# Kernel optimization log

Measured on AMD Instinct MI355X. Metric: run time of the kernel, lower is better.

## Reference

```python
import jax, jax.numpy as jnp
import numpy as np


def setup_inputs() -> dict:
    key = jax.random.key(0)
    k1, k2 = jax.random.split(key)
    D, N, M = 256, 1024, 1024
    z_x = jax.random.normal(k1, (1, D, N), dtype=jnp.float32)
    z_y = jax.random.normal(k2, (1, D, M), dtype=jnp.float32)
    return {"z_x": z_x, "z_y": z_y}


def reference(z_x, z_y):
    # squeeze().t(): (1, d, N) -> (N, d)
    x = jnp.squeeze(z_x).T  # (N, d)
    y = jnp.squeeze(z_y).T  # (M, d)
    # L1 compare: s[i, j] = -sum_d |x[i, d] - y[j, d]|  -> (N, M)
    s = -jnp.sum(jnp.abs(x[:, None, :] - y[None, :, :]), axis=-1)
    a = jax.nn.softmax(s, axis=1)  # row-wise softmax
    b = jax.nn.softmax(s, axis=0)  # column-wise softmax
    a = a + b - a * b              # soft union of alignments
    return jnp.sum(a * s) / jnp.sum(a)
```

## Files before the change

kernel.cpp:

```cpp
#include <hip/hip_runtime.h>
#include <math.h>


#define DD 256
#define NN 1024
#define NQ 256

__device__ __forceinline__ float waveMax(float v) {
  #pragma unroll
  for (int off = 32; off; off >>= 1) v = fmaxf(v, __shfl_xor(v, off, 64));
  return v;
}
__device__ __forceinline__ float waveSum(float v) {
  #pragma unroll
  for (int off = 32; off; off >>= 1) v += __shfl_xor(v, off, 64);
  return v;
}


__global__ __launch_bounds__(256, 1)
void scompute_kernel(const float* __restrict__ zx, const float* __restrict__ zy,
                     float* __restrict__ S,
                     float* __restrict__ pRM, float* __restrict__ pRL,
                     float* __restrict__ pCM, float* __restrict__ pCL) {
  const int bx = blockIdx.x;
  const int by = blockIdx.y;
  const int i0 = by * 16;
  const int t  = threadIdx.x;
  const int w  = t >> 6;
  const int ln = t & 63;

  __shared__ float xs[DD][16];
  __shared__ float ys[2][8][256];
  __shared__ float cmS[4][256];
  __shared__ float clS[4][256];

  const float4* __restrict__ X4 = (const float4*)zx;
  const float4* __restrict__ Y4 = (const float4*)zy;

  #pragma unroll
  for (int i = 0; i < 4; ++i) {
    const int k = t + i * 256;
    const int d = k >> 2, rq = k & 3;
    *(float4*)&xs[d][rq * 4] = X4[d * NQ + by * 4 + rq];
  }

  const int sd = t >> 6;
  const int sq = t & 63;
  {
    const float4 q0 = Y4[(sd)     * NQ + bx * 64 + sq];
    const float4 q1 = Y4[(4 + sd) * NQ + bx * 64 + sq];
    *(float4*)&ys[0][sd][sq * 4]     = q0;
    *(float4*)&ys[0][4 + sd][sq * 4] = q1;
  }
  __syncthreads();

  float acc[4][4];
  #pragma unroll
  for (int r = 0; r < 4; ++r)
    #pragma unroll
    for (int c = 0; c < 4; ++c) acc[r][c] = 0.f;

  #pragma unroll 1
  for (int n = 0; n < DD / 8; ++n) {
    const int buf = n & 1;
    float4 p0, p1;
    if (n < DD / 8 - 1) {
      p0 = Y4[(8 * (n + 1) + sd)     * NQ + bx * 64 + sq];
      p1 = Y4[(8 * (n + 1) + 4 + sd) * NQ + bx * 64 + sq];
    }
    #pragma unroll
    for (int dd = 0; dd < 8; ++dd) {
      const int d = n * 8 + dd;
      const float4 xv = *(const float4*)&xs[d][w * 4];
      const float4 yv = *(const float4*)&ys[buf][dd][ln * 4];
      acc[0][0] += fabsf(xv.x - yv.x); acc[0][1] += fabsf(xv.x - yv.y);
      acc[0][2] += fabsf(xv.x - yv.z); acc[0][3] += fabsf(xv.x - yv.w);
      acc[1][0] += fabsf(xv.y - yv.x); acc[1][1] += fabsf(xv.y - yv.y);
      acc[1][2] += fabsf(xv.y - yv.z); acc[1][3] += fabsf(xv.y - yv.w);
      acc[2][0] += fabsf(xv.z - yv.x); acc[2][1] += fabsf(xv.z - yv.y);
      acc[2][2] += fabsf(xv.z - yv.z); acc[2][3] += fabsf(xv.z - yv.w);
      acc[3][0] += fabsf(xv.w - yv.x); acc[3][1] += fabsf(xv.w - yv.y);
      acc[3][2] += fabsf(xv.w - yv.z); acc[3][3] += fabsf(xv.w - yv.w);
    }
    if (n < DD / 8 - 1) {
      *(float4*)&ys[buf ^ 1][sd][sq * 4]     = p0;
      *(float4*)&ys[buf ^ 1][4 + sd][sq * 4] = p1;
    }
    __syncthreads();
  }

  float4* __restrict__ S4 = (float4*)S;
  #pragma unroll
  for (int r = 0; r < 4; ++r)
    S4[(i0 + w * 4 + r) * NQ + bx * 64 + ln] =
        make_float4(acc[r][0], acc[r][1], acc[r][2], acc[r][3]);

  #pragma unroll
  for (int r = 0; r < 4; ++r) {
    float m = fmaxf(fmaxf(-acc[r][0], -acc[r][1]), fmaxf(-acc[r][2], -acc[r][3]));
    m = waveMax(m);
    float l = __expf(-acc[r][0] - m) + __expf(-acc[r][1] - m) +
              __expf(-acc[r][2] - m) + __expf(-acc[r][3] - m);
    l = waveSum(l);
    if (ln == 0) {
      pRM[bx * NN + i0 + w * 4 + r] = m;
      pRL[bx * NN + i0 + w * 4 + r] = l;
    }
  }

  #pragma unroll
  for (int c = 0; c < 4; ++c) {
    float m = fmaxf(fmaxf(-acc[0][c], -acc[1][c]), fmaxf(-acc[2][c], -acc[3][c]));
    float l = __expf(-acc[0][c] - m) + __expf(-acc[1][c] - m) +
              __expf(-acc[2][c] - m) + __expf(-acc[3][c] - m);
    cmS[w][ln * 4 + c] = m;
    clS[w][ln * 4 + c] = l;
  }
  __syncthreads();
  {
    const int j = t;
    const float m0 = cmS[0][j], m1 = cmS[1][j], m2 = cmS[2][j], m3 = cmS[3][j];
    const float M = fmaxf(fmaxf(m0, m1), fmaxf(m2, m3));
    const float L = clS[0][j] * __expf(m0 - M) + clS[1][j] * __expf(m1 - M) +
                    clS[2][j] * __expf(m2 - M) + clS[3][j] * __expf(m3 - M);
    pCM[by * NN + bx * 256 + j] = M;
    pCL[by * NN + bx * 256 + j] = L;
  }
}

__global__ __launch_bounds__(256)
void combine_kernel(const float* __restrict__ pRM, const float* __restrict__ pRL,
                    const float* __restrict__ pCM, const float* __restrict__ pCL,
                    float* __restrict__ rmax, float* __restrict__ rsum,
                    float* __restrict__ cmax, float* __restrict__ csum,
                    float* __restrict__ accum) {
  const int b = blockIdx.x, t = threadIdx.x;
  if (b == 0 && t == 0) {
    accum[0] = 0.f; accum[1] = 0.f; ((unsigned int*)accum)[2] = 0u;
  }
  if (b < 4) {
    const int r = b * 256 + t;
    float mk[4], lk[4];
    #pragma unroll
    for (int k = 0; k < 4; ++k) { mk[k] = pRM[k * NN + r]; lk[k] = pRL[k * NN + r]; }
    float m = fmaxf(fmaxf(mk[0], mk[1]), fmaxf(mk[2], mk[3]));
    float l = lk[0] * __expf(mk[0] - m) + lk[1] * __expf(mk[1] - m) +
              lk[2] * __expf(mk[2] - m) + lk[3] * __expf(mk[3] - m);
    rmax[r] = m; rsum[r] = l;
  } else {
    const int j = (b - 4) * 256 + t;
    float m = -1e30f;
    #pragma unroll 8
    for (int k = 0; k < 64; ++k) m = fmaxf(m, pCM[k * NN + j]);
    float l = 0.f;
    #pragma unroll 8
    for (int k = 0; k < 64; ++k) l += __expf(pCM[k * NN + j] - m) * pCL[k * NN + j];
    cmax[j] = m; csum[j] = l;
  }
}

__global__ __launch_bounds__(256)
void final_kernel(const float* __restrict__ S,
                  const float* __restrict__ rmax, const float* __restrict__ rsum,
                  const float* __restrict__ cmax, const float* __restrict__ csum,
                  float* __restrict__ accum, float* __restrict__ out) {
  __shared__ float redn[4], redd[4];
  const int t = threadIdx.x;
  const int row0 = blockIdx.x * 2;
  const float4* S4 = (const float4*)S;
  const float4 cm = ((const float4*)cmax)[t];
  const float4 cs = ((const float4*)csum)[t];
  float un = 0.f, ud = 0.f;
  #pragma unroll
  for (int r = 0; r < 2; ++r) {
    const int row = row0 + r;
    const float rm = rmax[row];
    const float ri = 1.f / rsum[row];
    const float4 p = S4[row * NQ + t];
    {
      const float s = -p.x;
      const float a = __expf(s - rm) * ri;
      const float b = __expf(s - cm.x) / cs.x;
      const float u = a + b - a * b;
      un += u * s; ud += u;
    }
    {
      const float s = -p.y;
      const float a = __expf(s - rm) * ri;
      const float b = __expf(s - cm.y) / cs.y;
      const float u = a + b - a * b;
      un += u * s; ud += u;
    }
    {
      const float s = -p.z;
      const float a = __expf(s - rm) * ri;
      const float b = __expf(s - cm.z) / cs.z;
      const float u = a + b - a * b;
      un += u * s; ud += u;
    }
    {
      const float s = -p.w;
      const float a = __expf(s - rm) * ri;
      const float b = __expf(s - cm.w) / cs.w;
      const float u = a + b - a * b;
      un += u * s; ud += u;
    }
  }
  un = waveSum(un); ud = waveSum(ud);
  if ((t & 63) == 0) { redn[t >> 6] = un; redd[t >> 6] = ud; }
  __syncthreads();
  if (t == 0) {
    atomicAdd(&accum[0], redn[0] + redn[1] + redn[2] + redn[3]);
    atomicAdd(&accum[1], redd[0] + redd[1] + redd[2] + redd[3]);
    __threadfence();
    unsigned int* cnt = (unsigned int*)accum + 2;
    const unsigned int old = atomicAdd(cnt, 1u);
    if (old == gridDim.x - 1) {
      const float n = atomicAdd(&accum[0], 0.f);
      const float d = atomicAdd(&accum[1], 0.f);
      out[0] = n / d;
    }
  }
}


#define TJ  128
#define NCH (NN / TJ)
#define BLK 256

__global__ __launch_bounds__(BLK)
void stats2_kernel(const float* __restrict__ zx, const float* __restrict__ zy,
                   float* __restrict__ partM, float* __restrict__ partS) {
  const int side = blockIdx.z;
  const float* __restrict__ X = side ? zy : zx;
  const float* __restrict__ Y = side ? zx : zy;
  const int j0 = blockIdx.x * TJ;
  const int i0 = blockIdx.y * 8;
  const int t  = threadIdx.x;
  const int rg = t >> 5;
  const int c  = t & 31;

  __shared__ float xs[8 * DD];
  for (int k = t; k < 8 * DD; k += BLK)
    xs[k] = X[(k >> 3) * NN + i0 + (k & 7)];
  __syncthreads();

  const float4* __restrict__ Y4 = (const float4*)Y;
  const int yb = (j0 >> 2) + c;
  float4 acc = make_float4(0.f, 0.f, 0.f, 0.f);
  #pragma unroll 8
  for (int d = 0; d < DD; ++d) {
    const float4 yv = Y4[d * NQ + yb];
    const float xv = xs[d * 8 + rg];
    acc.x += fabsf(xv - yv.x);
    acc.y += fabsf(xv - yv.y);
    acc.z += fabsf(xv - yv.z);
    acc.w += fabsf(xv - yv.w);
  }

  float m = fmaxf(fmaxf(-acc.x, -acc.y), fmaxf(-acc.z, -acc.w));
  #pragma unroll
  for (int off = 16; off > 0; off >>= 1) m = fmaxf(m, __shfl_xor(m, off, 32));
  float p = __expf(-acc.x - m) + __expf(-acc.y - m) +
            __expf(-acc.z - m) + __expf(-acc.w - m);
  #pragma unroll
  for (int off = 16; off > 0; off >>= 1) p += __shfl_xor(p, off, 32);

  if (c == 0) {
    const int idx = side * (NCH * NN) + blockIdx.x * NN + (i0 + rg);
    partM[idx] = m;
    partS[idx] = p;
  }
}

__global__ __launch_bounds__(BLK)
void combine_kernel_fb(const float* __restrict__ partM, const float* __restrict__ partS,
                       float* __restrict__ rmax, float* __restrict__ rsum,
                       float* __restrict__ cmax, float* __restrict__ csum,
                       float* __restrict__ accum) {
  const int gid = blockIdx.x * BLK + threadIdx.x;
  if (gid == 0) { accum[0] = 0.f; accum[1] = 0.f; }
  const int sd = gid >> 10;
  const int i  = gid & (NN - 1);
  float mk[NCH], sk[NCH];
  #pragma unroll
  for (int k = 0; k < NCH; ++k) {
    mk[k] = partM[sd * (NCH * NN) + k * NN + i];
    sk[k] = partS[sd * (NCH * NN) + k * NN + i];
  }
  float m = mk[0];
  #pragma unroll
  for (int k = 1; k < NCH; ++k) m = fmaxf(m, mk[k]);
  float s = 0.f;
  #pragma unroll
  for (int k = 0; k < NCH; ++k) s += __expf(mk[k] - m) * sk[k];
  if (sd == 0) { rmax[i] = m; rsum[i] = s; }
  else         { cmax[i] = m; csum[i] = s; }
}

__global__ __launch_bounds__(BLK)
void final2_kernel(const float* __restrict__ zx, const float* __restrict__ zy,
                   const float* __restrict__ rmax, const float* __restrict__ rsum,
                   const float* __restrict__ cmax, const float* __restrict__ csum,
                   float* __restrict__ accum) {
  const int j0 = blockIdx.x * TJ;
  const int i0 = blockIdx.y * 8;
  const int t  = threadIdx.x;
  const int rg = t >> 5;
  const int c  = t & 31;

  __shared__ float xs[8 * DD];
  __shared__ float redn[4], redd[4];
  for (int k = t; k < 8 * DD; k += BLK)
    xs[k] = zx[(k >> 3) * NN + i0 + (k & 7)];
  __syncthreads();

  const float4* __restrict__ Y4 = (const float4*)zy;
  const int yb = (j0 >> 2) + c;
  float4 acc = make_float4(0.f, 0.f, 0.f, 0.f);
  #pragma unroll 8
  for (int d = 0; d < DD; ++d) {
    const float4 yv = Y4[d * NQ + yb];
    const float xv = xs[d * 8 + rg];
    acc.x += fabsf(xv - yv.x);
    acc.y += fabsf(xv - yv.y);
    acc.z += fabsf(xv - yv.z);
    acc.w += fabsf(xv - yv.w);
  }

  const int i = i0 + rg;
  const float rm = rmax[i];
  const float ri = 1.f / rsum[i];
  const float4 cm = ((const float4*)cmax)[yb];
  const float4 cs = ((const float4*)csum)[yb];

  float un = 0.f, ud = 0.f;
  {
    const float s = -acc.x;
    const float a = __expf(s - rm) * ri;
    const float b = __expf(s - cm.x) / cs.x;
    const float u = a + b - a * b;
    un += u * s; ud += u;
  }
  {
    const float s = -acc.y;
    const float a = __expf(s - rm) * ri;
    const float b = __expf(s - cm.y) / cs.y;
    const float u = a + b - a * b;
    un += u * s; ud += u;
  }
  {
    const float s = -acc.z;
    const float a = __expf(s - rm) * ri;
    const float b = __expf(s - cm.z) / cs.z;
    const float u = a + b - a * b;
    un += u * s; ud += u;
  }
  {
    const float s = -acc.w;
    const float a = __expf(s - rm) * ri;
    const float b = __expf(s - cm.w) / cs.w;
    const float u = a + b - a * b;
    un += u * s; ud += u;
  }

  un = waveSum(un); ud = waveSum(ud);
  if ((t & 63) == 0) { redn[t >> 6] = un; redd[t >> 6] = ud; }
  __syncthreads();
  if (t == 0) {
    atomicAdd(&accum[0], redn[0] + redn[1] + redn[2] + redn[3]);
    atomicAdd(&accum[1], redd[0] + redd[1] + redd[2] + redd[3]);
  }
}

__global__ void finalize_kernel(const float* __restrict__ accum, float* __restrict__ out) {
  out[0] = accum[0] / accum[1];
}


extern "C" void kernel_launch(void* const* d_in, const int* in_sizes, int n_in,
                              void* d_out, int out_size, void* d_ws, size_t ws_size,
                              hipStream_t stream) {
  const float* zx = (const float*)d_in[0];
  const float* zy = (const float*)d_in[1];
  float* ws  = (float*)d_ws;
  float* out = (float*)d_out;

  float* accum = ws;
  float* S     = ws + 16;
  float* pRM   = S + NN * NN;
  float* pRL   = pRM + 4 * NN;
  float* pCM   = pRL + 4 * NN;
  float* pCL   = pCM + 64 * NN;
  float* rmax  = pCL + 64 * NN;
  float* rsum  = rmax + NN;
  float* cmax  = rsum + NN;
  float* csum  = cmax + NN;
  const size_t need = (size_t)((csum + NN) - ws) * sizeof(float);

  if (ws_size >= need) {
    dim3 g1(4, 64);
    scompute_kernel<<<g1, 256, 0, stream>>>(zx, zy, S, pRM, pRL, pCM, pCL);
    combine_kernel<<<8, 256, 0, stream>>>(pRM, pRL, pCM, pCL,
                                          rmax, rsum, cmax, csum, accum);
    final_kernel<<<NN / 2, 256, 0, stream>>>(S, rmax, rsum, cmax, csum, accum, out);
  } else {
    float* partM = ws + 16;
    float* partS = partM + 2 * NCH * NN;
    float* frmax = partS + 2 * NCH * NN;
    float* frsum = frmax + NN;
    float* fcmax = frsum + NN;
    float* fcsum = fcmax + NN;
    dim3 sgrid(NCH, NN / 8, 2);
    stats2_kernel<<<sgrid, BLK, 0, stream>>>(zx, zy, partM, partS);
    combine_kernel_fb<<<(2 * NN) / BLK, BLK, 0, stream>>>(partM, partS,
                                                          frmax, frsum, fcmax, fcsum, accum);
    dim3 fgrid(NCH, NN / 8);
    final2_kernel<<<fgrid, BLK, 0, stream>>>(zx, zy, frmax, frsum, fcmax, fcsum, accum);
    finalize_kernel<<<1, 1, 0, stream>>>(accum, out);
  }
}
```

Before: 127.8 us.

## Split feature dimension across two grid slices and move softmax stats to separate pass

The S computation now splits the 256-wide feature dimension into two halves via a z grid dimension, doubling the block count from 256 to 512 so more CUs are busy. Each half writes a partial S matrix. Row and column softmax statistics move out of the compute kernel into a new sumstats kernel that sums the two partials, with a new column-combine kernel. This costs an extra full S-sized buffer, extra global read/write traffic, and one more launch.

```diff
diff --git a/kernel.cpp b/kernel.cpp
--- a/kernel.cpp
+++ b/kernel.cpp
@@ -5,6 +5,7 @@
 #define DD 256
 #define NN 1024
 #define NQ 256
+#define HD 128
 
 __device__ __forceinline__ float waveMax(float v) {
   #pragma unroll
@@ -16,43 +17,51 @@
   for (int off = 32; off; off >>= 1) v += __shfl_xor(v, off, 64);
   return v;
 }
-
-
-__global__ __launch_bounds__(256, 1)
+__device__ __forceinline__ float blockMax(float v, float* red) {
+  v = waveMax(v);
+  __syncthreads();
+  if ((threadIdx.x & 63) == 0) red[threadIdx.x >> 6] = v;
+  __syncthreads();
+  return fmaxf(fmaxf(red[0], red[1]), fmaxf(red[2], red[3]));
+}
+__device__ __forceinline__ float blockSum(float v, float* red) {
+  v = waveSum(v);
+  __syncthreads();
+  if ((threadIdx.x & 63) == 0) red[threadIdx.x >> 6] = v;
+  __syncthreads();
+  return red[0] + red[1] + red[2] + red[3];
+}
+
+
+__global__ __launch_bounds__(256, 2)
 void scompute_kernel(const float* __restrict__ zx, const float* __restrict__ zy,
-                     float* __restrict__ S,
-                     float* __restrict__ pRM, float* __restrict__ pRL,
-                     float* __restrict__ pCM, float* __restrict__ pCL) {
+                     float* __restrict__ Sp) {
   const int bx = blockIdx.x;
   const int by = blockIdx.y;
+  const int h  = blockIdx.z;
   const int i0 = by * 16;
   const int t  = threadIdx.x;
   const int w  = t >> 6;
   const int ln = t & 63;
 
-  __shared__ float xs[DD][16];
+  __shared__ float xs[HD][16];
   __shared__ float ys[2][8][256];
-  __shared__ float cmS[4][256];
-  __shared__ float clS[4][256];
 
   const float4* __restrict__ X4 = (const float4*)zx;
   const float4* __restrict__ Y4 = (const float4*)zy;
 
   #pragma unroll
-  for (int i = 0; i < 4; ++i) {
+  for (int i = 0; i < 2; ++i) {
     const int k = t + i * 256;
     const int d = k >> 2, rq = k & 3;
-    *(float4*)&xs[d][rq * 4] = X4[d * NQ + by * 4 + rq];
-  }
-
-  const int sd = t >> 6;
-  const int sq = t & 63;
-  {
-    const float4 q0 = Y4[(sd)     * NQ + bx * 64 + sq];
-    const float4 q1 = Y4[(4 + sd) * NQ + bx * 64 + sq];
-    *(float4*)&ys[0][sd][sq * 4]     = q0;
-    *(float4*)&ys[0][4 + sd][sq * 4] = q1;
-  }
+    *(float4*)&xs[d][rq * 4] = X4[(h * HD + d) * NQ + by * 4 + rq];
+  }
+
+  const int sd = t >> 5;
+  const int sq = t & 31;
+  const int jq0 = bx * 64;
+  *(float4*)&ys[0][sd][sq * 4]        = Y4[(h * HD + sd) * NQ + jq0 + sq];
+  *(float4*)&ys[0][sd][(sq + 32) * 4] = Y4[(h * HD + sd) * NQ + jq0 + sq + 32];
   __syncthreads();
 
   float acc[4][4];
@@ -62,12 +71,12 @@
     for (int c = 0; c < 4; ++c) acc[r][c] = 0.f;
 
   #pragma unroll 1
-  for (int n = 0; n < DD / 8; ++n) {
+  for (int n = 0; n < HD / 8; ++n) {
     const int buf = n & 1;
     float4 p0, p1;
-    if (n < DD / 8 - 1) {
-      p0 = Y4[(8 * (n + 1) + sd)     * NQ + bx * 64 + sq];
-      p1 = Y4[(8 * (n + 1) + 4 + sd) * NQ + bx * 64 + sq];
+    if (n < HD / 8 - 1) {
+      p0 = Y4[(h * HD + 8 * (n + 1) + sd) * NQ + jq0 + sq];
+      p1 = Y4[(h * HD + 8 * (n + 1) + sd) * NQ + jq0 + sq + 32];
     }
     #pragma unroll
     for (int dd = 0; dd < 8; ++dd) {
@@ -83,92 +92,96 @@
       acc[3][0] += fabsf(xv.w - yv.x); acc[3][1] += fabsf(xv.w - yv.y);
       acc[3][2] += fabsf(xv.w - yv.z); acc[3][3] += fabsf(xv.w - yv.w);
     }
-    if (n < DD / 8 - 1) {
-      *(float4*)&ys[buf ^ 1][sd][sq * 4]     = p0;
-      *(float4*)&ys[buf ^ 1][4 + sd][sq * 4] = p1;
+    if (n < HD / 8 - 1) {
+      *(float4*)&ys[buf ^ 1][sd][sq * 4]        = p0;
+      *(float4*)&ys[buf ^ 1][sd][(sq + 32) * 4] = p1;
     }
     __syncthreads();
   }
 
-  float4* __restrict__ S4 = (float4*)S;
+  float4* __restrict__ S4 = (float4*)Sp + (size_t)h * (NN * NQ);
   #pragma unroll
   for (int r = 0; r < 4; ++r)
-    S4[(i0 + w * 4 + r) * NQ + bx * 64 + ln] =
+    S4[(i0 + w * 4 + r) * NQ + jq0 + ln] =
         make_float4(acc[r][0], acc[r][1], acc[r][2], acc[r][3]);
-
-  #pragma unroll
-  for (int r = 0; r < 4; ++r) {
-    float m = fmaxf(fmaxf(-acc[r][0], -acc[r][1]), fmaxf(-acc[r][2], -acc[r][3]));
-    m = waveMax(m);
-    float l = __expf(-acc[r][0] - m) + __expf(-acc[r][1] - m) +
-              __expf(-acc[r][2] - m) + __expf(-acc[r][3] - m);
-    l = waveSum(l);
-    if (ln == 0) {
-      pRM[bx * NN + i0 + w * 4 + r] = m;
-      pRL[bx * NN + i0 + w * 4 + r] = l;
-    }
-  }
-
-  #pragma unroll
-  for (int c = 0; c < 4; ++c) {
-    float m = fmaxf(fmaxf(-acc[0][c], -acc[1][c]), fmaxf(-acc[2][c], -acc[3][c]));
-    float l = __expf(-acc[0][c] - m) + __expf(-acc[1][c] - m) +
-              __expf(-acc[2][c] - m) + __expf(-acc[3][c] - m);
-    cmS[w][ln * 4 + c] = m;
-    clS[w][ln * 4 + c] = l;
-  }
-  __syncthreads();
-  {
-    const int j = t;
-    const float m0 = cmS[0][j], m1 = cmS[1][j], m2 = cmS[2][j], m3 = cmS[3][j];
-    const float M = fmaxf(fmaxf(m0, m1), fmaxf(m2, m3));
-    const float L = clS[0][j] * __expf(m0 - M) + clS[1][j] * __expf(m1 - M) +
-                    clS[2][j] * __expf(m2 - M) + clS[3][j] * __expf(m3 - M);
-    pCM[by * NN + bx * 256 + j] = M;
-    pCL[by * NN + bx * 256 + j] = L;
-  }
 }
 
 __global__ __launch_bounds__(256)
-void combine_kernel(const float* __restrict__ pRM, const float* __restrict__ pRL,
-                    const float* __restrict__ pCM, const float* __restrict__ pCL,
-                    float* __restrict__ rmax, float* __restrict__ rsum,
-                    float* __restrict__ cmax, float* __restrict__ csum,
-                    float* __restrict__ accum) {
+void sumstats_kernel(const float* __restrict__ Sp,
+                     float* __restrict__ rmax, float* __restrict__ rsum,
+                     float* __restrict__ pm, float* __restrict__ ps) {
+  __shared__ float red[4];
+  const int t = threadIdx.x;
+  const int row0 = blockIdx.x * 2;
+  const float4* A = (const float4*)Sp;
+  const float4* B = A + (size_t)NN * NQ;
+  float4 v[2];
+  #pragma unroll
+  for (int r = 0; r < 2; ++r) {
+    const float4 a = A[(row0 + r) * NQ + t];
+    const float4 b = B[(row0 + r) * NQ + t];
+    v[r] = make_float4(a.x + b.x, a.y + b.y, a.z + b.z, a.w + b.w);
+  }
+  #pragma unroll
+  for (int r = 0; r < 2; ++r) {
+    float m = fmaxf(fmaxf(-v[r].x, -v[r].y), fmaxf(-v[r].z, -v[r].w));
+    m = blockMax(m, red);
+    float l = __expf(-v[r].x - m) + __expf(-v[r].y - m) +
+              __expf(-v[r].z - m) + __expf(-v[r].w - m);
+    l = blockSum(l, red);
+    if (t == 0) { rmax[row0 + r] = m; rsum[row0 + r] = l; }
+  }
+  float4 cm, cl;
+  cm.x = fmaxf(-v[0].x, -v[1].x); cm.y = fmaxf(-v[0].y, -v[1].y);
+  cm.z = fmaxf(-v[0].z, -v[1].z); cm.w = fmaxf(-v[0].w, -v[1].w);
+  cl.x = __expf(-v[0].x - cm.x) + __expf(-v[1].x - cm.x);
+  cl.y = __expf(-v[0].y - cm.y) + __expf(-v[1].y - cm.y);
+  cl.z = __expf(-v[0].z - cm.z) + __expf(-v[1].z - cm.z);
+  cl.w = __expf(-v[0].w - cm.w) + __expf(-v[1].w - cm.w);
+  ((float4*)pm)[blockIdx.x * NQ + t] = cm;
+  ((float4*)ps)[blockIdx.x * NQ + t] = cl;
+}
+
+__global__ __launch_bounds__(256)
+void colcombine_kernel(const float* __restrict__ pm, const float* __restrict__ ps,
+                       float* __restrict__ cmax, float* __restrict__ csum,
+                       float* __restrict__ accum) {
+  __shared__ float sm[4][64], sl[4][64];
   const int b = blockIdx.x, t = threadIdx.x;
   if (b == 0 && t == 0) {
     accum[0] = 0.f; accum[1] = 0.f; ((unsigned int*)accum)[2] = 0u;
   }
-  if (b < 4) {
-    const int r = b * 256 + t;
-    float mk[4], lk[4];
-    #pragma unroll
-    for (int k = 0; k < 4; ++k) { mk[k] = pRM[k * NN + r]; lk[k] = pRL[k * NN + r]; }
-    float m = fmaxf(fmaxf(mk[0], mk[1]), fmaxf(mk[2], mk[3]));
-    float l = lk[0] * __expf(mk[0] - m) + lk[1] * __expf(mk[1] - m) +
-              lk[2] * __expf(mk[2] - m) + lk[3] * __expf(mk[3] - m);
-    rmax[r] = m; rsum[r] = l;
-  } else {
-    const int j = (b - 4) * 256 + t;
-    float m = -1e30f;
-    #pragma unroll 8
-    for (int k = 0; k < 64; ++k) m = fmaxf(m, pCM[k * NN + j]);
-    float l = 0.f;
-    #pragma unroll 8
-    for (int k = 0; k < 64; ++k) l += __expf(pCM[k * NN + j] - m) * pCL[k * NN + j];
-    cmax[j] = m; csum[j] = l;
+  const int c = t & 63;
+  const int g = t >> 6;
+  const int j = b * 64 + c;
+  float m = -1e30f;
+  #pragma unroll 8
+  for (int k = 0; k < 128; ++k) m = fmaxf(m, pm[(g * 128 + k) * NN + j]);
+  float l = 0.f;
+  #pragma unroll 8
+  for (int k = 0; k < 128; ++k)
+    l += __expf(pm[(g * 128 + k) * NN + j] - m) * ps[(g * 128 + k) * NN + j];
+  sm[g][c] = m; sl[g][c] = l;
+  __syncthreads();
+  if (g == 0) {
+    const float m0 = sm[0][c], m1 = sm[1][c], m2 = sm[2][c], m3 = sm[3][c];
+    const float M = fmaxf(fmaxf(m0, m1), fmaxf(m2, m3));
+    const float L = sl[0][c] * __expf(m0 - M) + sl[1][c] * __expf(m1 - M) +
+                    sl[2][c] * __expf(m2 - M) + sl[3][c] * __expf(m3 - M);
+    cmax[j] = M; csum[j] = L;
   }
 }
 
 __global__ __launch_bounds__(256)
-void final_kernel(const float* __restrict__ S,
+void final_kernel(const float* __restrict__ Sp,
                   const float* __restrict__ rmax, const float* __restrict__ rsum,
                   const float* __restrict__ cmax, const float* __restrict__ csum,
                   float* __restrict__ accum, float* __restrict__ out) {
   __shared__ float redn[4], redd[4];
   const int t = threadIdx.x;
   const int row0 = blockIdx.x * 2;
-  const float4* S4 = (const float4*)S;
+  const float4* A = (const float4*)Sp;
+  const float4* B = A + (size_t)NN * NQ;
   const float4 cm = ((const float4*)cmax)[t];
   const float4 cs = ((const float4*)csum)[t];
   float un = 0.f, ud = 0.f;
@@ -177,7 +190,9 @@
     const int row = row0 + r;
     const float rm = rmax[row];
     const float ri = 1.f / rsum[row];
-    const float4 p = S4[row * NQ + t];
+    const float4 pa = A[row * NQ + t];
+    const float4 pb = B[row * NQ + t];
+    const float4 p = make_float4(pa.x + pb.x, pa.y + pb.y, pa.z + pb.z, pa.w + pb.w);
     {
       const float s = -p.x;
       const float a = __expf(s - rm) * ri;
@@ -388,23 +403,21 @@
   float* out = (float*)d_out;
 
   float* accum = ws;
-  float* S     = ws + 16;
-  float* pRM   = S + NN * NN;
-  float* pRL   = pRM + 4 * NN;
-  float* pCM   = pRL + 4 * NN;
-  float* pCL   = pCM + 64 * NN;
-  float* rmax  = pCL + 64 * NN;
+  float* Sp    = ws + 16;
+  float* pm    = Sp + 2 * NN * NN;
+  float* ps    = pm + 512 * NN;
+  float* rmax  = ps + 512 * NN;
   float* rsum  = rmax + NN;
   float* cmax  = rsum + NN;
   float* csum  = cmax + NN;
   const size_t need = (size_t)((csum + NN) - ws) * sizeof(float);
 
   if (ws_size >= need) {
-    dim3 g1(4, 64);
-    scompute_kernel<<<g1, 256, 0, stream>>>(zx, zy, S, pRM, pRL, pCM, pCL);
-    combine_kernel<<<8, 256, 0, stream>>>(pRM, pRL, pCM, pCL,
-                                          rmax, rsum, cmax, csum, accum);
-    final_kernel<<<NN / 2, 256, 0, stream>>>(S, rmax, rsum, cmax, csum, accum, out);
+    dim3 g1(4, 64, 2);
+    scompute_kernel<<<g1, 256, 0, stream>>>(zx, zy, Sp);
+    sumstats_kernel<<<NN / 2, 256, 0, stream>>>(Sp, rmax, rsum, pm, ps);
+    colcombine_kernel<<<16, 256, 0, stream>>>(pm, ps, cmax, csum, accum);
+    final_kernel<<<NN / 2, 256, 0, stream>>>(Sp, rmax, rsum, cmax, csum, accum, out);
   } else {
     float* partM = ws + 16;
     float* partS = partM + 2 * NCH * NN;
```

Result: slower. 137.5 us (+7.6%).
